# Kernel tuning notes

Measured on AMD Instinct MI355X. Metric: run time of the kernel, lower is better.

The kernel has to match this reference:

```python
import jax, jax.numpy as jnp
import numpy as np
import math

B, L, D, H, FF = 2, 2048, 1024, 16, 4096
FACTOR = 5
EPS = 1e-5


def _ln(x, g, b):
    mu = jnp.mean(x, axis=-1, keepdims=True)
    var = jnp.mean((x - mu) ** 2, axis=-1, keepdims=True)
    return (x - mu) * jax.lax.rsqrt(var + EPS) * g + b


def setup_inputs() -> dict:
    key = jax.random.key(0)
    ks = jax.random.split(key, 16)
    s = D ** -0.5
    sample_k = min(FACTOR * int(np.ceil(np.log(L))), L)  # 40
    return {
        "x": jax.random.normal(ks[0], (B, L, D), jnp.float32),
        "Wq": jax.random.normal(ks[1], (D, D), jnp.float32) * s,
        "bq": jnp.zeros((D,), jnp.float32),
        "Wk": jax.random.normal(ks[2], (D, D), jnp.float32) * s,
        "bk": jnp.zeros((D,), jnp.float32),
        "Wv": jax.random.normal(ks[3], (D, D), jnp.float32) * s,
        "bv": jnp.zeros((D,), jnp.float32),
        "Wo": jax.random.normal(ks[4], (D, D), jnp.float32) * s,
        "bo": jnp.zeros((D,), jnp.float32),
        "ln1_g": jnp.ones((D,), jnp.float32),
        "ln1_b": jnp.zeros((D,), jnp.float32),
        "W1": jax.random.normal(ks[5], (D, FF), jnp.float32) * s,
        "b1": jnp.zeros((FF,), jnp.float32),
        "W2": jax.random.normal(ks[6], (FF, D), jnp.float32) * (FF ** -0.5),
        "b2": jnp.zeros((D,), jnp.float32),
        "ln2_g": jnp.ones((D,), jnp.float32),
        "ln2_b": jnp.zeros((D,), jnp.float32),
        "index_sample": jax.random.randint(ks[7], (L, sample_k), 0, L),
    }


def _prob_attn(Q, K, V, index_sample):
    # Q,K,V: [B,H,L,Dh]; Informer ProbAttention with mask_flag=True (causal).
    b, h, l, dh = Q.shape
    n_top = min(FACTOR * int(np.ceil(np.log(l))), l)
    # sampled scores: Q[l] . K[index_sample[l, s]]
    K_s = K[:, :, index_sample]                                  # [B,H,L,S,Dh]
    QKs = jnp.einsum("bhld,bhlsd->bhls", Q, K_s)                 # [B,H,L,S]
    M = QKs.max(-1) - QKs.sum(-1) / l                             # sparsity measure
    _, M_top = jax.lax.top_k(M, n_top)                            # [B,H,u]
    Q_red = jnp.take_along_axis(Q, M_top[..., None], axis=2)      # [B,H,u,Dh]
    scale = 1.0 / jnp.sqrt(jnp.asarray(dh, jnp.float32))
    scores = jnp.einsum("bhud,bhld->bhul", Q_red, K) * scale      # [B,H,u,L]
    causal = jnp.arange(l)[None, None, None, :] > M_top[..., None]
    scores = jnp.where(causal, -jnp.inf, scores)
    attn = jax.nn.softmax(scores, axis=-1)
    upd = jnp.einsum("bhul,bhld->bhud", attn, V)                  # [B,H,u,Dh]
    # initial context for masked case: running cumsum of V
    context = jnp.cumsum(V, axis=2)
    bi = jnp.arange(b)[:, None, None]
    hi = jnp.arange(h)[None, :, None]
    context = context.at[bi, hi, M_top].set(upd)
    return context                                               # [B,H,L,Dh]


def reference(x, Wq, bq, Wk, bk, Wv, bv, Wo, bo, ln1_g, ln1_b,
              W1, b1, W2, b2, ln2_g, ln2_b, index_sample):
    b, l, d = x.shape
    dh = d // H
    Q = (x @ Wq + bq).reshape(b, l, H, dh).transpose(0, 2, 1, 3)
    K = (x @ Wk + bk).reshape(b, l, H, dh).transpose(0, 2, 1, 3)
    V = (x @ Wv + bv).reshape(b, l, H, dh).transpose(0, 2, 1, 3)
    ctx = _prob_attn(Q, K, V, index_sample)
    ctx = ctx.transpose(0, 2, 1, 3).reshape(b, l, d)
    attn_out = ctx @ Wo + bo
    x1 = _ln(x + attn_out, ln1_g, ln1_b)
    ff = jnp.maximum(x1 @ W1 + b1, 0.0) @ W2 + b2
    return _ln(x1 + ff, ln2_g, ln2_b)
```

## Files before the change

kernel.cpp:

```cpp
#include <hip/hip_runtime.h>
#include <hip/hip_bf16.h>
#include <hip/hip_fp16.h>
#include <math.h>

constexpr int B = 2, L = 2048, D = 1024, H = 16, DH = 64, FFD = 4096;
constexpr int S = 40;
constexpr int U = 40;
constexpr float EPS = 1e-5f;
constexpr int NCHUNK = 32;
constexpr int CHLEN = L / NCHUNK;
constexpr int LD3 = 3 * D;
constexpr int LD2 = 2 * D;
constexpr int LDA2 = 2 * D;
constexpr int JT = 128;
constexpr int NJC = L / JT;

typedef __attribute__((ext_vector_type(8))) short short8;
typedef __attribute__((ext_vector_type(8))) _Float16 half8;
typedef __attribute__((ext_vector_type(4))) float f32x4;

__device__ __forceinline__ unsigned short f2bf(float v) {
  __hip_bfloat16 h = __float2bfloat16(v);
  return __builtin_bit_cast(unsigned short, h);
}
__device__ __forceinline__ float bf2f(unsigned short u) {
  unsigned int x = ((unsigned int)u) << 16;
  return __builtin_bit_cast(float, x);
}
__device__ __forceinline__ unsigned short f2h(float v) {
  __half h = __float2half(v);
  return __builtin_bit_cast(unsigned short, h);
}
__device__ __forceinline__ float h2f(unsigned short u) {
  return __half2float(__builtin_bit_cast(__half, u));
}

__device__ __forceinline__ void gload16(const void* g, void* l) {
  __builtin_amdgcn_global_load_lds(
      (const __attribute__((address_space(1))) void*)g,
      (__attribute__((address_space(3))) void*)l, 16, 0, 0);
}

template<bool RELU, bool OUT_BF16, bool F16, bool DUPA>
__global__ __launch_bounds__(256, 2) void gemm128_kernel(
    const unsigned short* __restrict__ A,
    const unsigned short* __restrict__ Bt,
    const float* __restrict__ bias,
    void* __restrict__ C, int M, int N, int K, int KA) {
  constexpr int GBM = 128, GBN = 128, GBK = 64;
  constexpr int ABUF = GBM * GBK;
  constexpr int BUFS = 2 * ABUF;
  __shared__ short lds[2 * BUFS];

  const int tid  = threadIdx.x;
  const int lane = tid & 63;
  const int wid  = tid >> 6;
  const int wr = wid >> 1;
  const int wc = wid & 1;

  const int nwg  = gridDim.x * gridDim.y;
  const int orig = blockIdx.y * gridDim.x + blockIdx.x;
  const int wg   = (orig & 7) * (nwg >> 3) + (orig >> 3);
  const int bm = (wg / gridDim.x) * GBM;
  const int bn = (wg % gridDim.x) * GBN;

  const int srow  = lane >> 3;
  const int sslot = (lane & 7) ^ srow;
  const unsigned short* aS = A  + (size_t)(bm + wid * 8 + srow) * KA + sslot * 8;
  const unsigned short* bS = Bt + (size_t)(bn + wid * 8 + srow) * K  + sslot * 8;
  short* la0 = lds + wid * 8 * GBK;
  short* lb0 = lds + ABUF + wid * 8 * GBK;

  auto STAGE = [&](int buf, int kt) {
    const int akt = (DUPA && kt >= 16) ? kt - 16 : kt;
    const unsigned short* ap = aS + (size_t)akt * GBK;
    const unsigned short* bp = bS + (size_t)kt  * GBK;
    short* la = la0 + buf * BUFS;
    short* lb = lb0 + buf * BUFS;
    gload16(ap,                   la);
    gload16(ap + (size_t)32 * KA, la + 32 * GBK);
    gload16(ap + (size_t)64 * KA, la + 64 * GBK);
    gload16(ap + (size_t)96 * KA, la + 96 * GBK);
    gload16(bp,                   lb);
    gload16(bp + (size_t)32 * K,  lb + 32 * GBK);
    gload16(bp + (size_t)64 * K,  lb + 64 * GBK);
    gload16(bp + (size_t)96 * K,  lb + 96 * GBK);
  };

  const int fr = lane & 15, g = lane >> 4;
  const int nt = K / GBK;

  STAGE(0, 0);

  f32x4 acc[4][4] = {};
  int cur = 0;
  for (int t = 0; t < nt; ++t) {
    const int kt = (t + 1 < nt) ? t + 1 : t;
    STAGE(cur ^ 1, kt);
    asm volatile("s_waitcnt vmcnt(8)" ::: "memory");
    __builtin_amdgcn_sched_barrier(0);
    __builtin_amdgcn_s_barrier();

    const short* la = lds + cur * BUFS;
    const short* lb = la + ABUF;
    short8 av[2][4], bv[2][4];
    #pragma unroll
    for (int kk = 0; kk < 2; ++kk) {
      #pragma unroll
      for (int mi = 0; mi < 4; ++mi) {
        const int row = wr * 64 + mi * 16 + fr;
        av[kk][mi] = *(const short8*)&la[row * GBK + ((((kk << 2) | g) ^ (fr & 7)) << 3)];
      }
      #pragma unroll
      for (int ni = 0; ni < 4; ++ni) {
        const int row = wc * 64 + ni * 16 + fr;
        bv[kk][ni] = *(const short8*)&lb[row * GBK + ((((kk << 2) | g) ^ (fr & 7)) << 3)];
      }
    }
    __builtin_amdgcn_s_setprio(1);
    #pragma unroll
    for (int kk = 0; kk < 2; ++kk)
      #pragma unroll
      for (int mi = 0; mi < 4; ++mi)
        #pragma unroll
        for (int ni = 0; ni < 4; ++ni) {
          if constexpr (F16)
            acc[mi][ni] = __builtin_amdgcn_mfma_f32_16x16x32_f16(
                __builtin_bit_cast(half8, av[kk][mi]),
                __builtin_bit_cast(half8, bv[kk][ni]), acc[mi][ni], 0, 0, 0);
          else
            acc[mi][ni] = __builtin_amdgcn_mfma_f32_16x16x32_bf16(
                av[kk][mi], bv[kk][ni], acc[mi][ni], 0, 0, 0);
        }
    __builtin_amdgcn_s_setprio(0);
    asm volatile("s_waitcnt lgkmcnt(0)" ::: "memory");
    __builtin_amdgcn_sched_barrier(0);
    __builtin_amdgcn_s_barrier();
    cur ^= 1;
  }

  #pragma unroll
  for (int ni = 0; ni < 4; ++ni) {
    const int col = bn + wc * 64 + ni * 16 + fr;
    const float bcol = bias[col];
    #pragma unroll
    for (int mi = 0; mi < 4; ++mi) {
      #pragma unroll
      for (int j = 0; j < 4; ++j) {
        const int rowg = bm + wr * 64 + mi * 16 + (g << 2) + j;
        float v = acc[mi][ni][j] + bcol;
        if (RELU) v = fmaxf(v, 0.f);
        if (OUT_BF16) ((unsigned short*)C)[(size_t)rowg * N + col] = f2bf(v);
        else          ((float*)C)[(size_t)rowg * N + col] = v;
      }
    }
  }
}

__global__ __launch_bounds__(256) void split_x_f16_kernel(
    const float* __restrict__ x, unsigned short* __restrict__ A2,
    unsigned short* __restrict__ xb) {
  const int i = (blockIdx.x * 256 + threadIdx.x) * 4;
  if (i >= B * L * D) return;
  const int m = i / D, k = i % D;
  const float4 v = *(const float4*)(x + i);
  ushort4 hi, lo, bb;
  hi.x = f2h(v.x); lo.x = f2h(v.x - h2f(hi.x)); bb.x = f2bf(v.x);
  hi.y = f2h(v.y); lo.y = f2h(v.y - h2f(hi.y)); bb.y = f2bf(v.y);
  hi.z = f2h(v.z); lo.z = f2h(v.z - h2f(hi.z)); bb.z = f2bf(v.z);
  hi.w = f2h(v.w); lo.w = f2h(v.w - h2f(hi.w)); bb.w = f2bf(v.w);
  unsigned short* row = A2 + (size_t)m * LDA2;
  *(ushort4*)(row + k)     = hi;
  *(ushort4*)(row + D + k) = lo;
  *(ushort4*)(xb + i) = bb;
}

__global__ __launch_bounds__(256) void wsplit_f16_kernel(
    const float* __restrict__ W, unsigned short* __restrict__ B2r) {
  __shared__ float tile[32][33];
  const int bx = blockIdx.x * 32;
  const int by = blockIdx.y * 32;
  const int tx = threadIdx.x & 31, ty = threadIdx.x >> 5;
  #pragma unroll
  for (int i = ty; i < 32; i += 8)
    tile[i][tx] = W[(size_t)(by + i) * D + bx + tx];
  __syncthreads();
  #pragma unroll
  for (int i = ty; i < 32; i += 8) {
    const float v = tile[tx][i];
    const unsigned short hi = f2h(v);
    const unsigned short lo = f2h(v - h2f(hi));
    unsigned short* r = B2r + (size_t)(bx + i) * LD3 + (by + tx);
    r[0]     = hi;
    r[D]     = lo;
    r[2 * D] = hi;
  }
}

__global__ __launch_bounds__(256) void transpose_bf16_kernel(
    const float* __restrict__ W, unsigned short* __restrict__ Wt, int K, int N) {
  __shared__ float tile[32][33];
  const int bx = blockIdx.x * 32;
  const int by = blockIdx.y * 32;
  const int tx = threadIdx.x & 31, ty = threadIdx.x >> 5;
  #pragma unroll
  for (int i = ty; i < 32; i += 8)
    tile[i][tx] = W[(size_t)(by + i) * N + bx + tx];
  __syncthreads();
  #pragma unroll
  for (int i = ty; i < 32; i += 8)
    Wt[(size_t)(bx + i) * K + by + tx] = f2bf(tile[tx][i]);
}

__global__ __launch_bounds__(256) void concat2_kernel(
    const float* __restrict__ a, const float* __restrict__ b, float* __restrict__ o) {
  const int i = blockIdx.x * 256 + threadIdx.x;
  if (i < D) o[i] = a[i];
  else if (i < 2 * D) o[i] = b[i - D];
}

__global__ __launch_bounds__(256) void prob_m_kernel(
    const float* __restrict__ QK, const int* __restrict__ idx,
    float* __restrict__ M_) {
  const int combo = blockIdx.x;
  const int b = combo >> 2, hg = combo & 3;
  const int l = blockIdx.y;
  const int tid = threadIdx.x;
  const int wave = tid >> 6;
  const int lane = tid & 63;
  const int h = hg * 4 + wave;
  __shared__ int sidx[S];
  if (tid < S) sidx[tid] = idx[l * S + tid];
  __syncthreads();
  const int dsub = (lane & 15) * 4;
  const int sgrp = lane >> 4;
  const float4 q = *(const float4*)(QK + ((size_t)b * L + l) * LD2 + h * DH + dsub);
  float mx = -INFINITY, sm = 0.f;
  for (int s = sgrp; s < S; s += 4) {
    const float4 kv = *(const float4*)(QK + ((size_t)b * L + sidx[s]) * LD2 + D + h * DH + dsub);
    float p = q.x*kv.x + q.y*kv.y + q.z*kv.z + q.w*kv.w;
    p += __shfl_xor(p, 1);
    p += __shfl_xor(p, 2);
    p += __shfl_xor(p, 4);
    p += __shfl_xor(p, 8);
    mx = fmaxf(mx, p);
    sm += p;
  }
  mx = fmaxf(mx, __shfl_xor(mx, 16));
  mx = fmaxf(mx, __shfl_xor(mx, 32));
  sm += __shfl_xor(sm, 16);
  sm += __shfl_xor(sm, 32);
  if (lane == 0)
    M_[((size_t)b * H + h) * L + l] = mx - sm / (float)L;
}

__global__ __launch_bounds__(64) void topk_kernel(
    const float* __restrict__ M_, int* __restrict__ Mtop) {
  const int bh = blockIdx.x;
  const float* row = M_ + (size_t)bh * L;
  const int lane = threadIdx.x;
  float v[32];
  #pragma unroll
  for (int k = 0; k < 32; ++k) v[k] = row[k * 64 + lane];
  for (int u = 0; u < U; ++u) {
    float best = v[0]; int bk = 0;
    #pragma unroll
    for (int k = 1; k < 32; ++k)
      if (v[k] > best) { best = v[k]; bk = k; }
    int bidx = bk * 64 + lane;
    #pragma unroll
    for (int off = 1; off < 64; off <<= 1) {
      const float ov = __shfl_xor(best, off);
      const int   oi = __shfl_xor(bidx, off);
      if (ov > best || (ov == best && oi < bidx)) { best = ov; bidx = oi; }
    }
    if (lane == 0) Mtop[bh * U + u] = bidx;
    if ((bidx & 63) == lane) {
      const int kk = bidx >> 6;
      #pragma unroll
      for (int k = 0; k < 32; ++k) if (k == kk) v[k] = -INFINITY;
    }
  }
}

__global__ __launch_bounds__(320) void attn_p1_kernel(
    const float* __restrict__ QK, const float* __restrict__ V,
    const int* __restrict__ Mtop,
    float* __restrict__ pmax, float* __restrict__ psum, float* __restrict__ pv) {
  const int jc = blockIdx.x, h = blockIdx.y, b = blockIdx.z;
  const int bh = b * H + h;
  const int tid = threadIdx.x;
  const int j0 = jc * JT;
  __shared__ float Qs[U][68];
  __shared__ float KVs[JT][68];
  __shared__ unsigned short ws[U][JT];

  for (int i = tid; i < U * 16; i += 320) {
    const int u = i >> 4, dq = (i & 15) << 2;
    const int row = Mtop[bh * U + u];
    *(float4*)&Qs[u][dq] =
        *(const float4*)(QK + ((size_t)b * L + row) * LD2 + h * DH + dq);
  }
  for (int i = tid; i < JT * 16; i += 320) {
    const int j = i >> 4, dq = (i & 15) << 2;
    *(float4*)&KVs[j][dq] =
        *(const float4*)(QK + ((size_t)b * L + j0 + j) * LD2 + D + h * DH + dq);
  }
  __syncthreads();

  const int u = tid >> 3, jg = tid & 7;
  const int mt = Mtop[bh * U + u];
  float sc[16];
  #pragma unroll
  for (int jt = 0; jt < 16; ++jt) sc[jt] = 0.f;
  for (int dq = 0; dq < 64; dq += 4) {
    const float4 q = *(const float4*)&Qs[u][dq];
    #pragma unroll
    for (int jt = 0; jt < 16; ++jt) {
      const float4 k = *(const float4*)&KVs[jt * 8 + jg][dq];
      sc[jt] += q.x*k.x + q.y*k.y + q.z*k.z + q.w*k.w;
    }
  }
  float m = -INFINITY;
  #pragma unroll
  for (int jt = 0; jt < 16; ++jt) {
    const int j = j0 + jt * 8 + jg;
    sc[jt] = (j <= mt) ? sc[jt] * 0.125f : -INFINITY;
    m = fmaxf(m, sc[jt]);
  }
  m = fmaxf(m, __shfl_xor(m, 1));
  m = fmaxf(m, __shfl_xor(m, 2));
  m = fmaxf(m, __shfl_xor(m, 4));
  float sum = 0.f;
  #pragma unroll
  for (int jt = 0; jt < 16; ++jt) {
    const float e = (sc[jt] == -INFINITY) ? 0.f : expf(sc[jt] - m);
    sum += e;
    ws[u][jt * 8 + jg] = f2bf(e);
  }
  sum += __shfl_xor(sum, 1);
  sum += __shfl_xor(sum, 2);
  sum += __shfl_xor(sum, 4);
  if (jg == 0) {
    pmax[(size_t)(bh * NJC + jc) * U + u] = m;
    psum[(size_t)(bh * NJC + jc) * U + u] = sum;
  }
  __syncthreads();
  for (int i = tid; i < JT * 16; i += 320) {
    const int j = i >> 4, dq = (i & 15) << 2;
    *(float4*)&KVs[j][dq] =
        *(const float4*)(V + ((size_t)b * L + j0 + j) * D + h * DH + dq);
  }
  __syncthreads();
  const int d = tid & 63, ug = tid >> 6;
  float acc[8] = {};
  for (int j = 0; j < JT; j += 2) {
    const float v0 = KVs[j][d], v1 = KVs[j + 1][d];
    #pragma unroll
    for (int k = 0; k < 8; ++k) {
      const int uu = ug + k * 5;
      const unsigned int wp = *(const unsigned int*)&ws[uu][j];
      acc[k] = fmaf(bf2f((unsigned short)(wp & 0xffff)), v0, acc[k]);
      acc[k] = fmaf(bf2f((unsigned short)(wp >> 16)), v1, acc[k]);
    }
  }
  #pragma unroll
  for (int k = 0; k < 8; ++k) {
    const int uu = ug + k * 5;
    pv[((size_t)(bh * NJC + jc) * U + uu) * DH + d] = acc[k];
  }
}

__global__ __launch_bounds__(64) void attn_p2_kernel(
    const float* __restrict__ pmax, const float* __restrict__ psum,
    const float* __restrict__ pv, const int* __restrict__ Mtop,
    unsigned short* __restrict__ ctx16) {
  const int bid = blockIdx.x;
  const int u = bid % U, bh = bid / U;
  const int d = threadIdx.x;
  float gmax = -INFINITY;
  for (int c = 0; c < NJC; ++c)
    gmax = fmaxf(gmax, pmax[(size_t)(bh * NJC + c) * U + u]);
  float den = 0.f, num = 0.f;
  for (int c = 0; c < NJC; ++c) {
    const float m = pmax[(size_t)(bh * NJC + c) * U + u];
    if (m == -INFINITY) continue;
    const float s = expf(m - gmax);
    den += psum[(size_t)(bh * NJC + c) * U + u] * s;
    num += pv[((size_t)(bh * NJC + c) * U + u) * DH + d] * s;
  }
  const int h = bh % H, b = bh / H;
  const int l = Mtop[bh * U + u];
  ctx16[((size_t)b * L + l) * D + h * DH + d] = f2bf(num / den);
}

__global__ __launch_bounds__(256) void cumsum_pass1(
    const float* __restrict__ V, float* __restrict__ ctx, float* __restrict__ csums) {
  const int c = blockIdx.x * 256 + threadIdx.x;
  const int ch = blockIdx.y, b = blockIdx.z;
  size_t base = ((size_t)b * L + (size_t)ch * CHLEN) * D + c;
  float acc = 0.f;
  for (int i = 0; i < CHLEN; ++i) {
    const size_t o = base + (size_t)i * D;
    acc += V[o];
    ctx[o] = acc;
  }
  csums[((size_t)b * NCHUNK + ch) * D + c] = acc;
}

__global__ __launch_bounds__(256) void cumsum_pass2(
    const float* __restrict__ ctx, const float* __restrict__ csums,
    unsigned short* __restrict__ ctx16) {
  const int c = blockIdx.x * 256 + threadIdx.x;
  const int ch = blockIdx.y, b = blockIdx.z;
  float off = 0.f;
  for (int j = 0; j < ch; ++j) off += csums[((size_t)b * NCHUNK + j) * D + c];
  size_t base = ((size_t)b * L + (size_t)ch * CHLEN) * D + c;
  for (int i = 0; i < CHLEN; ++i) {
    const size_t o = base + (size_t)i * D;
    ctx16[o] = f2bf(ctx[o] + off);
  }
}

__global__ __launch_bounds__(256) void add_ln_kernel(
    const float* __restrict__ a, const float* __restrict__ r,
    const float* __restrict__ g, const float* __restrict__ be,
    float* __restrict__ out, unsigned short* __restrict__ out16) {
  const int row = blockIdx.x;
  const int tid = threadIdx.x;
  __shared__ float buf[D];
  __shared__ float red[256];
  const float* pa = a + (size_t)row * D;
  const float* pr = r + (size_t)row * D;
  float s = 0.f;
  for (int i = tid; i < D; i += 256) { float v = pa[i] + pr[i]; buf[i] = v; s += v; }
  red[tid] = s; __syncthreads();
  for (int off = 128; off > 0; off >>= 1) {
    if (tid < off) red[tid] += red[tid+off];
    __syncthreads();
  }
  const float mu = red[0] / (float)D;
  __syncthreads();
  float s2 = 0.f;
  for (int i = tid; i < D; i += 256) { float dv = buf[i] - mu; s2 += dv * dv; }
  red[tid] = s2; __syncthreads();
  for (int off = 128; off > 0; off >>= 1) {
    if (tid < off) red[tid] += red[tid+off];
    __syncthreads();
  }
  const float rstd = rsqrtf(red[0] / (float)D + EPS);
  __syncthreads();
  float* po = out + (size_t)row * D;
  for (int i = tid; i < D; i += 256) {
    float v = (buf[i] - mu) * rstd * g[i] + be[i];
    po[i] = v;
    if (out16) out16[(size_t)row * D + i] = f2bf(v);
  }
}

extern "C" void kernel_launch(void* const* d_in, const int* in_sizes, int n_in,
                              void* d_out, int out_size, void* d_ws, size_t ws_size,
                              hipStream_t stream) {
  const float* x   = (const float*)d_in[0];
  const float* Wq  = (const float*)d_in[1];
  const float* bq  = (const float*)d_in[2];
  const float* Wk  = (const float*)d_in[3];
  const float* bk  = (const float*)d_in[4];
  const float* Wv  = (const float*)d_in[5];
  const float* bv  = (const float*)d_in[6];
  const float* Wo  = (const float*)d_in[7];
  const float* bo  = (const float*)d_in[8];
  const float* g1  = (const float*)d_in[9];
  const float* be1 = (const float*)d_in[10];
  const float* W1  = (const float*)d_in[11];
  const float* b1  = (const float*)d_in[12];
  const float* W2  = (const float*)d_in[13];
  const float* b2  = (const float*)d_in[14];
  const float* g2  = (const float*)d_in[15];
  const float* be2 = (const float*)d_in[16];
  const int*   idx = (const int*)d_in[17];
  float* out = (float*)d_out;

  char* p = (char*)d_ws;
  unsigned short* A2   = (unsigned short*)p;
  float*          ctxb = (float*)p;
  float*          AO   = (float*)p;
  float*          ff2  = (float*)p;
  unsigned short* xb    = (unsigned short*)(p + 16777216);
  unsigned short* ctx16 = (unsigned short*)(p + 16777216);
  unsigned short* B2 = (unsigned short*)(p + 25165824);
  char* scr = p + 25165824;
  float* Mbuf   = (float*)(scr);
  float* csum   = (float*)(scr + 262144);
  int*   Mtop   = (int*)  (scr + 524288);
  float* pmax   = (float*)(scr + 532480);
  float* psum   = (float*)(scr + 614400);
  float* pv     = (float*)(scr + 696320);
  float*          QKb = (float*)(p + 37748736);
  float*          x1  = (float*)(p + 37748736);
  unsigned short* x1b = (unsigned short*)(p + 54525952);
  unsigned short* ff1b = (unsigned short*)(p + 62914560);
  float* Vb = (float*)(p + 96468992);
  unsigned short* Wvt = (unsigned short*)(p + 113246208);
  unsigned short* Wot = (unsigned short*)(p + 115343360);
  unsigned short* W1t = (unsigned short*)(p + 117440512);
  unsigned short* W2t = (unsigned short*)(p + 125829120);
  float* qkbias = (float*)(p + 134217728);

  dim3 blk(256);
  const int M = B * L;
  const int SZ = B * L * D;

  split_x_f16_kernel<<<(SZ/4 + 255)/256, blk, 0, stream>>>(x, A2, xb);
  wsplit_f16_kernel<<<dim3(D/32, D/32), blk, 0, stream>>>(Wq, B2);
  wsplit_f16_kernel<<<dim3(D/32, D/32), blk, 0, stream>>>(Wk, B2 + (size_t)D * LD3);
  concat2_kernel<<<8, blk, 0, stream>>>(bq, bk, qkbias);
  gemm128_kernel<false,false,true,true><<<dim3(LD2/128, M/128), blk, 0, stream>>>(
      A2, B2, qkbias, QKb, M, LD2, LD3, LDA2);
  transpose_bf16_kernel<<<dim3(D/32,  D/32),   blk, 0, stream>>>(Wv, Wvt, D, D);
  transpose_bf16_kernel<<<dim3(D/32,  D/32),   blk, 0, stream>>>(Wo, Wot, D, D);
  transpose_bf16_kernel<<<dim3(FFD/32, D/32),  blk, 0, stream>>>(W1, W1t, D, FFD);
  transpose_bf16_kernel<<<dim3(D/32,  FFD/32), blk, 0, stream>>>(W2, W2t, FFD, D);
  gemm128_kernel<false,false,false,false><<<dim3(D/128, M/128), blk, 0, stream>>>(
      xb, Wvt, bv, Vb, M, D, D, D);
  prob_m_kernel<<<dim3(8, L), blk, 0, stream>>>(QKb, idx, Mbuf);
  topk_kernel<<<B*H, dim3(64), 0, stream>>>(Mbuf, Mtop);
  attn_p1_kernel<<<dim3(NJC, H, B), dim3(320), 0, stream>>>(QKb, Vb, Mtop, pmax, psum, pv);
  cumsum_pass1<<<dim3(D/256, NCHUNK, B), blk, 0, stream>>>(Vb, ctxb, csum);
  cumsum_pass2<<<dim3(D/256, NCHUNK, B), blk, 0, stream>>>(ctxb, csum, ctx16);
  attn_p2_kernel<<<B*H*U, dim3(64), 0, stream>>>(pmax, psum, pv, Mtop, ctx16);
  gemm128_kernel<false,false,false,false><<<dim3(D/128, M/128), blk, 0, stream>>>(
      ctx16, Wot, bo, AO, M, D, D, D);
  add_ln_kernel<<<B*L, blk, 0, stream>>>(x, AO, g1, be1, x1, x1b);
  gemm128_kernel<true,true,false,false><<<dim3(FFD/128, M/128), blk, 0, stream>>>(
      x1b, W1t, b1, ff1b, M, FFD, D, D);
  gemm128_kernel<false,false,false,false><<<dim3(D/128, M/128), blk, 0, stream>>>(
      ff1b, W2t, b2, ff2, M, D, FFD, FFD);
  add_ln_kernel<<<B*L, blk, 0, stream>>>(x1, ff2, g2, be2, out,
                                         (unsigned short*)nullptr);
}
```

Measured before the change: 384.7 us.

## Use 128x64 GEMM tiles for N=1024 GEMMs, merge transposes, drop fp32 x1

The GEMM is templated on N-tile width and occupancy. The three GEMMs with N=1024 now use 128x64 tiles at 3 blocks per CU, which doubles their grid from 256 to 512 workgroups and fills more of the CU array. The four weight transposes are merged into one launch, and the bias-concat kernel is removed by picking bq/bk in the QK GEMM epilogue. The fp32 x1 buffer is no longer written; the second layernorm reads the bf16 copy x1b as its residual, which lowers residual precision in exchange for less memory traffic.

```diff
diff --git a/kernel.cpp b/kernel.cpp
--- a/kernel.cpp
+++ b/kernel.cpp
@@ -41,15 +41,19 @@
       (__attribute__((address_space(3))) void*)l, 16, 0, 0);
 }
 
-template<bool RELU, bool OUT_BF16, bool F16, bool DUPA>
-__global__ __launch_bounds__(256, 2) void gemm128_kernel(
+template<int GBN, int MINB, bool RELU, bool OUT_BF16, bool F16, bool DUPA>
+__global__ __launch_bounds__(256, MINB) void gemm_kernel(
     const unsigned short* __restrict__ A,
     const unsigned short* __restrict__ Bt,
     const float* __restrict__ bias,
+    const float* __restrict__ biasB,
     void* __restrict__ C, int M, int N, int K, int KA) {
-  constexpr int GBM = 128, GBN = 128, GBK = 64;
+  constexpr int GBM = 128, GBK = 64;
   constexpr int ABUF = GBM * GBK;
-  constexpr int BUFS = 2 * ABUF;
+  constexpr int BBUF = GBN * GBK;
+  constexpr int BUFS = ABUF + BBUF;
+  constexpr int NI = GBN / 32;
+  constexpr int NLOADS = 4 + GBN / 32;
   __shared__ short lds[2 * BUFS];
 
   const int tid  = threadIdx.x;
@@ -81,10 +85,9 @@
     gload16(ap + (size_t)32 * KA, la + 32 * GBK);
     gload16(ap + (size_t)64 * KA, la + 64 * GBK);
     gload16(ap + (size_t)96 * KA, la + 96 * GBK);
-    gload16(bp,                   lb);
-    gload16(bp + (size_t)32 * K,  lb + 32 * GBK);
-    gload16(bp + (size_t)64 * K,  lb + 64 * GBK);
-    gload16(bp + (size_t)96 * K,  lb + 96 * GBK);
+    #pragma unroll
+    for (int r = 0; r < GBN / 32; ++r)
+      gload16(bp + (size_t)(r * 32) * K, lb + r * 32 * GBK);
   };
 
   const int fr = lane & 15, g = lane >> 4;
@@ -92,18 +95,21 @@
 
   STAGE(0, 0);
 
-  f32x4 acc[4][4] = {};
+  f32x4 acc[4][NI] = {};
   int cur = 0;
   for (int t = 0; t < nt; ++t) {
     const int kt = (t + 1 < nt) ? t + 1 : t;
     STAGE(cur ^ 1, kt);
-    asm volatile("s_waitcnt vmcnt(8)" ::: "memory");
+    if constexpr (NLOADS == 8)
+      asm volatile("s_waitcnt vmcnt(8)" ::: "memory");
+    else
+      asm volatile("s_waitcnt vmcnt(6)" ::: "memory");
     __builtin_amdgcn_sched_barrier(0);
     __builtin_amdgcn_s_barrier();
 
     const short* la = lds + cur * BUFS;
     const short* lb = la + ABUF;
-    short8 av[2][4], bv[2][4];
+    short8 av[2][4], bv[2][NI];
     #pragma unroll
     for (int kk = 0; kk < 2; ++kk) {
       #pragma unroll
@@ -112,8 +118,8 @@
         av[kk][mi] = *(const short8*)&la[row * GBK + ((((kk << 2) | g) ^ (fr & 7)) << 3)];
       }
       #pragma unroll
-      for (int ni = 0; ni < 4; ++ni) {
-        const int row = wc * 64 + ni * 16 + fr;
+      for (int ni = 0; ni < NI; ++ni) {
+        const int row = wc * (GBN / 2) + ni * 16 + fr;
         bv[kk][ni] = *(const short8*)&lb[row * GBK + ((((kk << 2) | g) ^ (fr & 7)) << 3)];
       }
     }
@@ -123,7 +129,7 @@
       #pragma unroll
       for (int mi = 0; mi < 4; ++mi)
         #pragma unroll
-        for (int ni = 0; ni < 4; ++ni) {
+        for (int ni = 0; ni < NI; ++ni) {
           if constexpr (F16)
             acc[mi][ni] = __builtin_amdgcn_mfma_f32_16x16x32_f16(
                 __builtin_bit_cast(half8, av[kk][mi]),
@@ -140,9 +146,9 @@
   }
 
   #pragma unroll
-  for (int ni = 0; ni < 4; ++ni) {
-    const int col = bn + wc * 64 + ni * 16 + fr;
-    const float bcol = bias[col];
+  for (int ni = 0; ni < NI; ++ni) {
+    const int col = bn + wc * (GBN / 2) + ni * 16 + fr;
+    const float bcol = DUPA ? (col < D ? bias[col] : biasB[col - D]) : bias[col];
     #pragma unroll
     for (int mi = 0; mi < 4; ++mi) {
       #pragma unroll
@@ -197,11 +203,21 @@
   }
 }
 
-__global__ __launch_bounds__(256) void transpose_bf16_kernel(
-    const float* __restrict__ W, unsigned short* __restrict__ Wt, int K, int N) {
+__global__ __launch_bounds__(256) void transpose4_bf16_kernel(
+    const float* __restrict__ Wv, const float* __restrict__ Wo,
+    const float* __restrict__ W1, const float* __restrict__ W2,
+    unsigned short* __restrict__ Wvt, unsigned short* __restrict__ Wot,
+    unsigned short* __restrict__ W1t, unsigned short* __restrict__ W2t) {
+  const int bid = blockIdx.x;
+  const float* W; unsigned short* Wt; int K, N, t;
+  if (bid < 1024)      { W = Wv; Wt = Wvt; K = D;   N = D;   t = bid; }
+  else if (bid < 2048) { W = Wo; Wt = Wot; K = D;   N = D;   t = bid - 1024; }
+  else if (bid < 6144) { W = W1; Wt = W1t; K = D;   N = FFD; t = bid - 2048; }
+  else                 { W = W2; Wt = W2t; K = FFD; N = D;   t = bid - 6144; }
+  const int nx = N / 32;
+  const int bx = (t % nx) * 32;
+  const int by = (t / nx) * 32;
   __shared__ float tile[32][33];
-  const int bx = blockIdx.x * 32;
-  const int by = blockIdx.y * 32;
   const int tx = threadIdx.x & 31, ty = threadIdx.x >> 5;
   #pragma unroll
   for (int i = ty; i < 32; i += 8)
@@ -210,13 +226,6 @@
   #pragma unroll
   for (int i = ty; i < 32; i += 8)
     Wt[(size_t)(bx + i) * K + by + tx] = f2bf(tile[tx][i]);
-}
-
-__global__ __launch_bounds__(256) void concat2_kernel(
-    const float* __restrict__ a, const float* __restrict__ b, float* __restrict__ o) {
-  const int i = blockIdx.x * 256 + threadIdx.x;
-  if (i < D) o[i] = a[i];
-  else if (i < 2 * D) o[i] = b[i - D];
 }
 
 __global__ __launch_bounds__(256) void prob_m_kernel(
@@ -422,18 +431,24 @@
   }
 }
 
+template<bool ABF16>
 __global__ __launch_bounds__(256) void add_ln_kernel(
-    const float* __restrict__ a, const float* __restrict__ r,
+    const void* __restrict__ a_, const float* __restrict__ r,
     const float* __restrict__ g, const float* __restrict__ be,
     float* __restrict__ out, unsigned short* __restrict__ out16) {
   const int row = blockIdx.x;
   const int tid = threadIdx.x;
   __shared__ float buf[D];
   __shared__ float red[256];
-  const float* pa = a + (size_t)row * D;
   const float* pr = r + (size_t)row * D;
   float s = 0.f;
-  for (int i = tid; i < D; i += 256) { float v = pa[i] + pr[i]; buf[i] = v; s += v; }
+  for (int i = tid; i < D; i += 256) {
+    float av;
+    if (ABF16) av = bf2f(((const unsigned short*)a_)[(size_t)row * D + i]);
+    else       av = ((const float*)a_)[(size_t)row * D + i];
+    float v = av + pr[i];
+    buf[i] = v; s += v;
+  }
   red[tid] = s; __syncthreads();
   for (int off = 128; off > 0; off >>= 1) {
     if (tid < off) red[tid] += red[tid+off];
@@ -450,10 +465,9 @@
   }
   const float rstd = rsqrtf(red[0] / (float)D + EPS);
   __syncthreads();
-  float* po = out + (size_t)row * D;
   for (int i = tid; i < D; i += 256) {
     float v = (buf[i] - mu) * rstd * g[i] + be[i];
-    po[i] = v;
+    if (out)   out[(size_t)row * D + i] = v;
     if (out16) out16[(size_t)row * D + i] = f2bf(v);
   }
 }
@@ -497,7 +511,6 @@
   float* psum   = (float*)(scr + 614400);
   float* pv     = (float*)(scr + 696320);
   float*          QKb = (float*)(p + 37748736);
-  float*          x1  = (float*)(p + 37748736);
   unsigned short* x1b = (unsigned short*)(p + 54525952);
   unsigned short* ff1b = (unsigned short*)(p + 62914560);
   float* Vb = (float*)(p + 96468992);
@@ -505,7 +518,6 @@
   unsigned short* Wot = (unsigned short*)(p + 115343360);
   unsigned short* W1t = (unsigned short*)(p + 117440512);
   unsigned short* W2t = (unsigned short*)(p + 125829120);
-  float* qkbias = (float*)(p + 134217728);
 
   dim3 blk(256);
   const int M = B * L;
@@ -514,28 +526,24 @@
   split_x_f16_kernel<<<(SZ/4 + 255)/256, blk, 0, stream>>>(x, A2, xb);
   wsplit_f16_kernel<<<dim3(D/32, D/32), blk, 0, stream>>>(Wq, B2);
   wsplit_f16_kernel<<<dim3(D/32, D/32), blk, 0, stream>>>(Wk, B2 + (size_t)D * LD3);
-  concat2_kernel<<<8, blk, 0, stream>>>(bq, bk, qkbias);
-  gemm128_kernel<false,false,true,true><<<dim3(LD2/128, M/128), blk, 0, stream>>>(
-      A2, B2, qkbias, QKb, M, LD2, LD3, LDA2);
-  transpose_bf16_kernel<<<dim3(D/32,  D/32),   blk, 0, stream>>>(Wv, Wvt, D, D);
-  transpose_bf16_kernel<<<dim3(D/32,  D/32),   blk, 0, stream>>>(Wo, Wot, D, D);
-  transpose_bf16_kernel<<<dim3(FFD/32, D/32),  blk, 0, stream>>>(W1, W1t, D, FFD);
-  transpose_bf16_kernel<<<dim3(D/32,  FFD/32), blk, 0, stream>>>(W2, W2t, FFD, D);
-  gemm128_kernel<false,false,false,false><<<dim3(D/128, M/128), blk, 0, stream>>>(
-      xb, Wvt, bv, Vb, M, D, D, D);
+  gemm_kernel<128,2,false,false,true,true><<<dim3(LD2/128, M/128), blk, 0, stream>>>(
+      A2, B2, bq, bk, QKb, M, LD2, LD3, LDA2);
+  transpose4_bf16_kernel<<<10240, blk, 0, stream>>>(Wv, Wo, W1, W2, Wvt, Wot, W1t, W2t);
+  gemm_kernel<64,3,false,false,false,false><<<dim3(D/64, M/128), blk, 0, stream>>>(
+      xb, Wvt, bv, bv, Vb, M, D, D, D);
   prob_m_kernel<<<dim3(8, L), blk, 0, stream>>>(QKb, idx, Mbuf);
   topk_kernel<<<B*H, dim3(64), 0, stream>>>(Mbuf, Mtop);
   attn_p1_kernel<<<dim3(NJC, H, B), dim3(320), 0, stream>>>(QKb, Vb, Mtop, pmax, psum, pv);
   cumsum_pass1<<<dim3(D/256, NCHUNK, B), blk, 0, stream>>>(Vb, ctxb, csum);
   cumsum_pass2<<<dim3(D/256, NCHUNK, B), blk, 0, stream>>>(ctxb, csum, ctx16);
   attn_p2_kernel<<<B*H*U, dim3(64), 0, stream>>>(pmax, psum, pv, Mtop, ctx16);
-  gemm128_kernel<false,false,false,false><<<dim3(D/128, M/128), blk, 0, stream>>>(
-      ctx16, Wot, bo, AO, M, D, D, D);
-  add_ln_kernel<<<B*L, blk, 0, stream>>>(x, AO, g1, be1, x1, x1b);
-  gemm128_kernel<true,true,false,false><<<dim3(FFD/128, M/128), blk, 0, stream>>>(
-      x1b, W1t, b1, ff1b, M, FFD, D, D);
-  gemm128_kernel<false,false,false,false><<<dim3(D/128, M/128), blk, 0, stream>>>(
-      ff1b, W2t, b2, ff2, M, D, FFD, FFD);
-  add_ln_kernel<<<B*L, blk, 0, stream>>>(x1, ff2, g2, be2, out,
-                                         (unsigned short*)nullptr);
-}
+  gemm_kernel<64,3,false,false,false,false><<<dim3(D/64, M/128), blk, 0, stream>>>(
+      ctx16, Wot, bo, bo, AO, M, D, D, D);
+  add_ln_kernel<false><<<B*L, blk, 0, stream>>>(x, AO, g1, be1, nullptr, x1b);
+  gemm_kernel<128,2,true,true,false,false><<<dim3(FFD/128, M/128), blk, 0, stream>>>(
+      x1b, W1t, b1, b1, ff1b, M, FFD, D, D);
+  gemm_kernel<64,3,false,false,false,false><<<dim3(D/64, M/128), blk, 0, stream>>>(
+      ff1b, W2t, b2, b2, ff2, M, D, FFD, FFD);
+  add_ln_kernel<true><<<B*L, blk, 0, stream>>>(x1b, ff2, g2, be2, out,
+                                               (unsigned short*)nullptr);
+}
```

Measured after the change: 366.8 us. -4.6%, faster.
